# Kernel optimization log

Hardware: AMD Instinct MI355X
Metric: run time of the kernel (lower is better)

The kernel has to match this reference:

```python
import jax, jax.numpy as jnp
import numpy as np


def setup_inputs() -> dict:
    key = jax.random.key(0)
    k1, k2 = jax.random.split(key)
    B, T, D = 8, 2048, 2048
    layer_in = jax.random.normal(k1, (B, T, D), dtype=jnp.float32)
    # nn.Linear(2D, 2D): weight [out=2D, in=2D], bias [2D]
    W_gate = jax.random.normal(k2, (2 * D, 2 * D), dtype=jnp.float32) * 0.02
    b_gate = jnp.zeros((2 * D,), dtype=jnp.float32)
    return {"layer_in": layer_in, "W_gate": W_gate, "b_gate": b_gate}


def reference(layer_in, W_gate, b_gate):
    # Cumulative average: tril(ones)/row_index @ x  ==  cumsum(x)/[1..t]
    t = layer_in.shape[1]
    denom = jnp.arange(1, t + 1, dtype=layer_in.dtype)[:, None]  # (t, 1)
    average_out = jnp.cumsum(layer_in, axis=1) / denom  # (B, t, D)
    # Gating: Linear(2D -> 2D) on concat(x, avg), then chunk into two gates
    gating_in = jnp.concatenate([layer_in, average_out], axis=-1)  # (B, t, 2D)
    gates = jnp.einsum('btk,ok->bto', gating_in, W_gate) + b_gate  # (B, t, 2D)
    input_gate, forget_gate = jnp.split(gates, 2, axis=2)
    gating_out = (jax.nn.sigmoid(input_gate) * layer_in
                  + jax.nn.sigmoid(forget_gate) * average_out)
    return gating_out, average_out
```

## Files before the change

### kernel.cpp

```cpp
#include <hip/hip_runtime.h>
#include <hip/hip_bf16.h>


#define Bb 8
#define Tt 2048
#define Dd 2048
#define Mm (Bb * Tt)
#define Kk 4096
#define NTK 128
#define NC 32
#define CT 64

typedef __bf16 bf16x8 __attribute__((ext_vector_type(8)));
typedef float f32x16 __attribute__((ext_vector_type(16)));

__device__ __forceinline__ void gload16(const void* g, void* l) {
    __builtin_amdgcn_global_load_lds(
        (const __attribute__((address_space(1))) unsigned int*)g,
        (__attribute__((address_space(3))) unsigned int*)l, 16, 0, 0);
}

__global__ void wconv_kernel(const float* __restrict__ W,
                             unsigned short* __restrict__ Wb, long n) {
    long i = ((long)blockIdx.x * blockDim.x + threadIdx.x) * 4;
    long stride = (long)gridDim.x * blockDim.x * 4;
    for (; i < n; i += stride) {
        float4 v = *(const float4*)(W + i);
        __hip_bfloat16 a = __float2bfloat16(v.x);
        __hip_bfloat16 b = __float2bfloat16(v.y);
        __hip_bfloat16 c = __float2bfloat16(v.z);
        __hip_bfloat16 d = __float2bfloat16(v.w);
        ushort4 u;
        u.x = *(unsigned short*)&a; u.y = *(unsigned short*)&b;
        u.z = *(unsigned short*)&c; u.w = *(unsigned short*)&d;
        *(ushort4*)(Wb + i) = u;
    }
}

__global__ void ksum_kernel(const float* __restrict__ X, float* __restrict__ S) {
    int d = blockIdx.y * 256 + threadIdx.x;
    int bc = blockIdx.x;
    int b = bc >> 5, c = bc & 31;
    const float* p = X + ((long)(b * Tt + c * CT)) * Dd + d;
    float s = 0.f;
#pragma unroll 8
    for (int t = 0; t < CT; ++t) s += p[(long)t * Dd];
    S[(long)bc * Dd + d] = s;
}

__global__ void kscan_kernel(const float* __restrict__ X, const float* __restrict__ S,
                             float* __restrict__ AVG, unsigned short* __restrict__ Gin) {
    int d = blockIdx.y * 256 + threadIdx.x;
    int bc = blockIdx.x;
    int b = bc >> 5, c = bc & 31;
    const float* Sp = S + (long)(b * NC) * Dd + d;
    float run = 0.f;
    for (int cc = 0; cc < c; ++cc) run += Sp[(long)cc * Dd];
    const float* p = X + ((long)(b * Tt + c * CT)) * Dd + d;
    long row = (long)b * Tt + c * CT;
    for (int tt = 0; tt < CT; ++tt) {
        float x = p[(long)tt * Dd];
        run += x;
        float av = run / (float)(c * CT + tt + 1);
        long r = row + tt;
        AVG[r * Dd + d] = av;
        __hip_bfloat16 xb = __float2bfloat16(x);
        __hip_bfloat16 ab = __float2bfloat16(av);
        Gin[r * 4096 + d] = *(unsigned short*)&xb;
        Gin[r * 4096 + 2048 + d] = *(unsigned short*)&ab;
    }
}

#define MFMA32(va, vb, c_) c_ = __builtin_amdgcn_mfma_f32_32x32x16_bf16(va, vb, c_, 0, 0, 0)
#define RD(p_, i_) (*(const bf16x8*)((p_) + (i_) * 2048))

#define PH(t_, kk_, IA_, IB_)                                                   \
  {                                                                             \
    const int buf_ = (t_) & 3;                                                  \
    const char* pa_ = ((kk_) ? rA1 : rA0) + buf_ * 32768;                       \
    const char* pb_ = ((kk_) ? rB1 : rB0) + buf_ * 32768;                       \
    bf16x8 a0 = RD(pa_,0), a1 = RD(pa_,1), a2 = RD(pa_,2), a3 = RD(pa_,3);      \
    bf16x8 b0 = RD(pb_,0), b1 = RD(pb_,1);                                      \
    if (IA_) { char* nd_ = ldsb + (((t_)+3)&3)*32768 + woff;                    \
      const long ko_ = ((long)(t_)+3)*64;                                       \
      gload16(gA0 + ko_, nd_); gload16(gA1 + ko_, nd_ + 8192); }                \
    if (IB_) { char* nd_ = ldsb + (((t_)+3)&3)*32768 + 16384 + woff;            \
      const long ko_ = ((long)(t_)+3)*64;                                       \
      gload16(gB0 + ko_, nd_); gload16(gB1 + ko_, nd_ + 8192); }                \
    __builtin_amdgcn_s_barrier();                                               \
    __builtin_amdgcn_sched_barrier(0);                                          \
    __builtin_amdgcn_s_setprio(1);                                              \
    MFMA32(a0, b0, acc[0][0]); MFMA32(a0, b1, acc[0][1]);                       \
    MFMA32(a1, b0, acc[1][0]); MFMA32(a1, b1, acc[1][1]);                       \
    MFMA32(a2, b0, acc[2][0]); MFMA32(a2, b1, acc[2][1]);                       \
    MFMA32(a3, b0, acc[3][0]); MFMA32(a3, b1, acc[3][1]);                       \
    __builtin_amdgcn_s_setprio(0);                                              \
    __builtin_amdgcn_sched_barrier(0);                                          \
  }

#define BOUNDARY(N_)                                                            \
  asm volatile("s_waitcnt vmcnt(" #N_ ")" ::: "memory");                        \
  __builtin_amdgcn_s_barrier();                                                 \
  __builtin_amdgcn_sched_barrier(0);

__global__ __launch_bounds__(512, 2) void gemm32_kernel(
    const unsigned short* __restrict__ Gin,
    const unsigned short* __restrict__ Wb,
    const float* __restrict__ bias,
    const float* __restrict__ X,
    const float* __restrict__ AVG,
    float* __restrict__ OUT)
{
    __shared__ __attribute__((aligned(128))) char lds[131072];
    char* ldsb = (char*)lds;

    const int tid = threadIdx.x;
    const int w = tid >> 6, l = tid & 63;
    const int wm = w >> 2, wn = w & 3;
    const int la = l & 31;
    const int lk = l >> 5;
    const int woff = w * 1024;

    const int bid = blockIdx.x;
    const int batch = bid >> 8;
    const int rr = bid & 255;
    const int xcd = rr & 7;
    const int j = rr >> 3;
    const int nt = xcd * 2 + (j >> 4);
    const int mt = batch * 16 + (j & 15);
    const long m0 = (long)mt * 256;
    const int n0 = nt * 128;

    const int srow = tid >> 2;
    const int schunk = (tid & 3) ^ ((tid >> 3) & 3);
    const char* gA0 = (const char*)Gin + (m0 + srow) * 8192 + schunk * 16;
    const char* gA1 = gA0 + 128 * 8192;
    const long jr0 = n0 + ((srow >> 6) << 5) + (srow & 31) + (((srow >> 5) & 1) << 11);
    const int j1 = 128 + srow;
    const long jr1 = n0 + ((j1 >> 6) << 5) + (j1 & 31) + (((j1 >> 5) & 1) << 11);
    const char* gB0 = (const char*)Wb + jr0 * 8192 + schunk * 16;
    const char* gB1 = (const char*)Wb + jr1 * 8192 + schunk * 16;

    const int cb0 = ((lk ^ ((la >> 1) & 3))) * 16;
    const int cb1 = cb0 ^ 32;
    const char* rA0 = ldsb + (wm * 128 + la) * 64 + cb0;
    const char* rA1 = ldsb + (wm * 128 + la) * 64 + cb1;
    const char* rB0 = ldsb + 16384 + (wn * 64 + la) * 64 + cb0;
    const char* rB1 = ldsb + 16384 + (wn * 64 + la) * 64 + cb1;

    f32x16 acc[4][2] = {};

    {
        gload16(gA0,       ldsb + woff);
        gload16(gA1,       ldsb + 8192 + woff);
        gload16(gB0,       ldsb + 16384 + woff);
        gload16(gB1,       ldsb + 24576 + woff);
        gload16(gA0 + 64,  ldsb + 32768 + woff);
        gload16(gA1 + 64,  ldsb + 32768 + 8192 + woff);
        gload16(gB0 + 64,  ldsb + 32768 + 16384 + woff);
        gload16(gB1 + 64,  ldsb + 32768 + 24576 + woff);
        gload16(gA0 + 128, ldsb + 65536 + woff);
        gload16(gA1 + 128, ldsb + 65536 + 8192 + woff);
        gload16(gB0 + 128, ldsb + 65536 + 16384 + woff);
        gload16(gB1 + 128, ldsb + 65536 + 24576 + woff);
    }
    BOUNDARY(8);

#pragma unroll 1
    for (int t = 0; t < NTK - 3; ++t) {
        PH(t, 0, 1, 0);
        PH(t, 1, 0, 1);
        BOUNDARY(8);
    }
    PH(125, 0, 0, 0); PH(125, 1, 0, 0);
    BOUNDARY(4);
    PH(126, 0, 0, 0); PH(126, 1, 0, 0);
    BOUNDARY(0);
    PH(127, 0, 0, 0); PH(127, 1, 0, 0);

    const int d = n0 + wn * 32 + la;
    const float bi_ = bias[d];
    const float bf_ = bias[d + 2048];
#pragma unroll
    for (int mi = 0; mi < 4; ++mi) {
        const long rb = m0 + wm * 128 + mi * 32 + lk * 4;
        f32x16 ci = acc[mi][0];
        f32x16 cf = acc[mi][1];
#pragma unroll
        for (int q = 0; q < 16; ++q) {
            long row = rb + (q & 3) + 8 * (q >> 2);
            long idx = row * 2048 + d;
            float gi = ci[q] + bi_;
            float gf = cf[q] + bf_;
            float x = X[idx];
            float av = AVG[idx];
            float si = 1.f / (1.f + __expf(-gi));
            float sf = 1.f / (1.f + __expf(-gf));
            OUT[idx] = si * x + sf * av;
        }
    }
}

extern "C" void kernel_launch(void* const* d_in, const int* in_sizes, int n_in,
                              void* d_out, int out_size, void* d_ws, size_t ws_size,
                              hipStream_t stream) {
    const float* X = (const float*)d_in[0];
    const float* W = (const float*)d_in[1];
    const float* bias = (const float*)d_in[2];

    float* OUT = (float*)d_out;
    float* AVG = OUT + (long)Mm * Dd;

    char* ws = (char*)d_ws;
    unsigned short* Wb  = (unsigned short*)ws;
    unsigned short* Gin = (unsigned short*)(ws + 33554432);
    float* S = (float*)(ws + 33554432 + 134217728);

    wconv_kernel<<<2048, 256, 0, stream>>>(W, Wb, (long)Kk * Kk);
    ksum_kernel<<<dim3(Bb * NC, Dd / 256), 256, 0, stream>>>(X, S);
    kscan_kernel<<<dim3(Bb * NC, Dd / 256), 256, 0, stream>>>(X, S, AVG, Gin);
    gemm32_kernel<<<1024, 512, 0, stream>>>(Gin, Wb, bias, X, AVG, OUT);
}
```

Baseline: 690.0 us.

## Load B operand directly into registers, shrink LDS to 3-stage A buffer

The GEMM kernel stops staging the weight (B) tiles through LDS. Each wave now loads its B fragments straight from global memory into double-buffered registers one k-step ahead, and only the activation (A) tile goes through a 3-deep LDS ring. LDS use drops from 128KB to 48KB and the loop is unrolled by 6 with one barrier per k-tile. The aim is to cut LDS traffic and barriers and to allow more occupancy. The cost is that B global loads are no longer shared across the 2 waves that use the same B rows, which raises global and L2 traffic, and global latency is only hidden one step ahead.

```diff
diff --git a/kernel.cpp b/kernel.cpp
--- a/kernel.cpp
+++ b/kernel.cpp
@@ -74,36 +74,46 @@
 #define MFMA32(va, vb, c_) c_ = __builtin_amdgcn_mfma_f32_32x32x16_bf16(va, vb, c_, 0, 0, 0)
 #define RD(p_, i_) (*(const bf16x8*)((p_) + (i_) * 2048))
 
-#define PH(t_, kk_, IA_, IB_)                                                   \
+#define TILE(t_, buf_, bs_, IB_, IA_, NV_)                                      \
   {                                                                             \
-    const int buf_ = (t_) & 3;                                                  \
-    const char* pa_ = ((kk_) ? rA1 : rA0) + buf_ * 32768;                       \
-    const char* pb_ = ((kk_) ? rB1 : rB0) + buf_ * 32768;                       \
-    bf16x8 a0 = RD(pa_,0), a1 = RD(pa_,1), a2 = RD(pa_,2), a3 = RD(pa_,3);      \
-    bf16x8 b0 = RD(pb_,0), b1 = RD(pb_,1);                                      \
-    if (IA_) { char* nd_ = ldsb + (((t_)+3)&3)*32768 + woff;                    \
-      const long ko_ = ((long)(t_)+3)*64;                                       \
-      gload16(gA0 + ko_, nd_); gload16(gA1 + ko_, nd_ + 8192); }                \
-    if (IB_) { char* nd_ = ldsb + (((t_)+3)&3)*32768 + 16384 + woff;            \
-      const long ko_ = ((long)(t_)+3)*64;                                       \
-      gload16(gB0 + ko_, nd_); gload16(gB1 + ko_, nd_ + 8192); }                \
+    if (IB_) {                                                                  \
+      const long o_ = ((long)(t_) + 1) * 64;                                    \
+      breg[(bs_) ^ 1][0] = *(const bf16x8*)(pB0 + o_);                          \
+      breg[(bs_) ^ 1][1] = *(const bf16x8*)(pB0 + o_ + 32);                     \
+      breg[(bs_) ^ 1][2] = *(const bf16x8*)(pB1 + o_);                          \
+      breg[(bs_) ^ 1][3] = *(const bf16x8*)(pB1 + o_ + 32);                     \
+    }                                                                           \
+    if (IA_) {                                                                  \
+      char* nd_ = ldsb + (((t_) + 2) % 3) * 16384 + woff;                       \
+      const long ko_ = ((long)(t_) + 2) * 64;                                   \
+      gload16(gA0 + ko_, nd_); gload16(gA1 + ko_, nd_ + 8192);                  \
+    }                                                                           \
+    {                                                                           \
+      const char* pa_ = rA0 + (buf_) * 16384;                                   \
+      bf16x8 a0 = RD(pa_,0), a1 = RD(pa_,1), a2 = RD(pa_,2), a3 = RD(pa_,3);    \
+      __builtin_amdgcn_s_setprio(1);                                            \
+      MFMA32(a0, breg[bs_][0], acc[0][0]); MFMA32(a0, breg[bs_][2], acc[0][1]); \
+      MFMA32(a1, breg[bs_][0], acc[1][0]); MFMA32(a1, breg[bs_][2], acc[1][1]); \
+      MFMA32(a2, breg[bs_][0], acc[2][0]); MFMA32(a2, breg[bs_][2], acc[2][1]); \
+      MFMA32(a3, breg[bs_][0], acc[3][0]); MFMA32(a3, breg[bs_][2], acc[3][1]); \
+      __builtin_amdgcn_s_setprio(0);                                            \
+    }                                                                           \
+    {                                                                           \
+      const char* pa_ = rA1 + (buf_) * 16384;                                   \
+      bf16x8 a0 = RD(pa_,0), a1 = RD(pa_,1), a2 = RD(pa_,2), a3 = RD(pa_,3);    \
+      __builtin_amdgcn_s_setprio(1);                                            \
+      MFMA32(a0, breg[bs_][1], acc[0][0]); MFMA32(a0, breg[bs_][3], acc[0][1]); \
+      MFMA32(a1, breg[bs_][1], acc[1][0]); MFMA32(a1, breg[bs_][3], acc[1][1]); \
+      MFMA32(a2, breg[bs_][1], acc[2][0]); MFMA32(a2, breg[bs_][3], acc[2][1]); \
+      MFMA32(a3, breg[bs_][1], acc[3][0]); MFMA32(a3, breg[bs_][3], acc[3][1]); \
+      __builtin_amdgcn_s_setprio(0);                                            \
+    }                                                                           \
+    asm volatile("s_waitcnt vmcnt(" #NV_ ")" ::: "memory");                     \
     __builtin_amdgcn_s_barrier();                                               \
     __builtin_amdgcn_sched_barrier(0);                                          \
-    __builtin_amdgcn_s_setprio(1);                                              \
-    MFMA32(a0, b0, acc[0][0]); MFMA32(a0, b1, acc[0][1]);                       \
-    MFMA32(a1, b0, acc[1][0]); MFMA32(a1, b1, acc[1][1]);                       \
-    MFMA32(a2, b0, acc[2][0]); MFMA32(a2, b1, acc[2][1]);                       \
-    MFMA32(a3, b0, acc[3][0]); MFMA32(a3, b1, acc[3][1]);                       \
-    __builtin_amdgcn_s_setprio(0);                                              \
-    __builtin_amdgcn_sched_barrier(0);                                          \
   }
 
-#define BOUNDARY(N_)                                                            \
-  asm volatile("s_waitcnt vmcnt(" #N_ ")" ::: "memory");                        \
-  __builtin_amdgcn_s_barrier();                                                 \
-  __builtin_amdgcn_sched_barrier(0);
-
-__global__ __launch_bounds__(512, 2) void gemm32_kernel(
+__global__ __launch_bounds__(512, 2) void gemm32r_kernel(
     const unsigned short* __restrict__ Gin,
     const unsigned short* __restrict__ Wb,
     const float* __restrict__ bias,
@@ -111,7 +121,7 @@
     const float* __restrict__ AVG,
     float* __restrict__ OUT)
 {
-    __shared__ __attribute__((aligned(128))) char lds[131072];
+    __shared__ __attribute__((aligned(128))) char lds[49152];
     char* ldsb = (char*)lds;
 
     const int tid = threadIdx.x;
@@ -135,48 +145,41 @@
     const int schunk = (tid & 3) ^ ((tid >> 3) & 3);
     const char* gA0 = (const char*)Gin + (m0 + srow) * 8192 + schunk * 16;
     const char* gA1 = gA0 + 128 * 8192;
-    const long jr0 = n0 + ((srow >> 6) << 5) + (srow & 31) + (((srow >> 5) & 1) << 11);
-    const int j1 = 128 + srow;
-    const long jr1 = n0 + ((j1 >> 6) << 5) + (j1 & 31) + (((j1 >> 5) & 1) << 11);
-    const char* gB0 = (const char*)Wb + jr0 * 8192 + schunk * 16;
-    const char* gB1 = (const char*)Wb + jr1 * 8192 + schunk * 16;
+
+    const char* pB0 = (const char*)Wb + (long)(n0 + wn * 32 + la) * 8192 + lk * 16;
+    const char* pB1 = (const char*)Wb + (long)(n0 + wn * 32 + la + 2048) * 8192 + lk * 16;
 
     const int cb0 = ((lk ^ ((la >> 1) & 3))) * 16;
     const int cb1 = cb0 ^ 32;
     const char* rA0 = ldsb + (wm * 128 + la) * 64 + cb0;
     const char* rA1 = ldsb + (wm * 128 + la) * 64 + cb1;
-    const char* rB0 = ldsb + 16384 + (wn * 64 + la) * 64 + cb0;
-    const char* rB1 = ldsb + 16384 + (wn * 64 + la) * 64 + cb1;
 
     f32x16 acc[4][2] = {};
-
-    {
-        gload16(gA0,       ldsb + woff);
-        gload16(gA1,       ldsb + 8192 + woff);
-        gload16(gB0,       ldsb + 16384 + woff);
-        gload16(gB1,       ldsb + 24576 + woff);
-        gload16(gA0 + 64,  ldsb + 32768 + woff);
-        gload16(gA1 + 64,  ldsb + 32768 + 8192 + woff);
-        gload16(gB0 + 64,  ldsb + 32768 + 16384 + woff);
-        gload16(gB1 + 64,  ldsb + 32768 + 24576 + woff);
-        gload16(gA0 + 128, ldsb + 65536 + woff);
-        gload16(gA1 + 128, ldsb + 65536 + 8192 + woff);
-        gload16(gB0 + 128, ldsb + 65536 + 16384 + woff);
-        gload16(gB1 + 128, ldsb + 65536 + 24576 + woff);
-    }
-    BOUNDARY(8);
+    bf16x8 breg[2][4];
+
+    gload16(gA0,      ldsb + woff);
+    gload16(gA1,      ldsb + 8192 + woff);
+    gload16(gA0 + 64, ldsb + 16384 + woff);
+    gload16(gA1 + 64, ldsb + 16384 + 8192 + woff);
+    breg[0][0] = *(const bf16x8*)(pB0);
+    breg[0][1] = *(const bf16x8*)(pB0 + 32);
+    breg[0][2] = *(const bf16x8*)(pB1);
+    breg[0][3] = *(const bf16x8*)(pB1 + 32);
+    asm volatile("s_waitcnt vmcnt(0)" ::: "memory");
+    __builtin_amdgcn_s_barrier();
+    __builtin_amdgcn_sched_barrier(0);
 
 #pragma unroll 1
-    for (int t = 0; t < NTK - 3; ++t) {
-        PH(t, 0, 1, 0);
-        PH(t, 1, 0, 1);
-        BOUNDARY(8);
-    }
-    PH(125, 0, 0, 0); PH(125, 1, 0, 0);
-    BOUNDARY(4);
-    PH(126, 0, 0, 0); PH(126, 1, 0, 0);
-    BOUNDARY(0);
-    PH(127, 0, 0, 0); PH(127, 1, 0, 0);
+    for (int t = 0; t < 126; t += 6) {
+        TILE(t + 0, 0, 0, 1, 1, 2)
+        TILE(t + 1, 1, 1, 1, 1, 2)
+        TILE(t + 2, 2, 0, 1, 1, 2)
+        TILE(t + 3, 0, 1, 1, 1, 2)
+        TILE(t + 4, 1, 0, 1, 1, 2)
+        TILE(t + 5, 2, 1, 1, 1, 2)
+    }
+    TILE(126, 0, 0, 1, 0, 0)
+    TILE(127, 1, 1, 0, 0, 0)
 
     const int d = n0 + wn * 32 + la;
     const float bi_ = bias[d];
@@ -219,5 +222,5 @@
     wconv_kernel<<<2048, 256, 0, stream>>>(W, Wb, (long)Kk * Kk);
     ksum_kernel<<<dim3(Bb * NC, Dd / 256), 256, 0, stream>>>(X, S);
     kscan_kernel<<<dim3(Bb * NC, Dd / 256), 256, 0, stream>>>(X, S, AVG, Gin);
-    gemm32_kernel<<<1024, 512, 0, stream>>>(Gin, Wb, bias, X, AVG, OUT);
-}
+    gemm32r_kernel<<<1024, 512, 0, stream>>>(Gin, Wb, bias, X, AVG, OUT);
+}
```

New measurement: 998.5 us. 44.7% more time.

## Restructure GEMM main loop to double-buffered K=128 tiles with register ping-pong

Applied to the files above, without the earlier changes.

The GEMM pipeline changes from a 4-deep ring of K=64 LDS stages to two 64KB buffers holding K=128 tiles, with one barrier per tile. LDS fragment reads are ping-ponged between two register sets so the next reads overlap the current MFMA cluster. The epilogue now reads the bf16 copies of x and avg from Gin instead of the fp32 X and AVG arrays, which halves epilogue read traffic but loses precision in the output blend. Launch bounds drop the 2-blocks hint, and each tile now waits for vmcnt(0), so prefetch depth is reduced.

```diff
diff --git a/kernel.cpp b/kernel.cpp
--- a/kernel.cpp
+++ b/kernel.cpp
@@ -7,7 +7,6 @@
 #define Dd 2048
 #define Mm (Bb * Tt)
 #define Kk 4096
-#define NTK 128
 #define NC 32
 #define CT 64
 
@@ -72,43 +71,69 @@
 }
 
 #define MFMA32(va, vb, c_) c_ = __builtin_amdgcn_mfma_f32_32x32x16_bf16(va, vb, c_, 0, 0, 0)
-#define RD(p_, i_) (*(const bf16x8*)((p_) + (i_) * 2048))
-
-#define PH(t_, kk_, IA_, IB_)                                                   \
+#define SBAR __builtin_amdgcn_s_barrier()
+#define SCHB __builtin_amdgcn_sched_barrier(0)
+#define LGKM0 do { asm volatile("s_waitcnt lgkmcnt(0)" ::: "memory"); SCHB; } while (0)
+
+#define READ6(S_, pA_, pB_)                                                     \
+    S_##a0 = *(const bf16x8*)(pA_);                                             \
+    S_##a1 = *(const bf16x8*)((pA_) + 4096);                                    \
+    S_##a2 = *(const bf16x8*)((pA_) + 8192);                                    \
+    S_##a3 = *(const bf16x8*)((pA_) + 12288);                                   \
+    S_##b0 = *(const bf16x8*)(pB_);                                             \
+    S_##b1 = *(const bf16x8*)((pB_) + 4096);
+
+#define CLUST(S_)                                                               \
+    __builtin_amdgcn_s_setprio(1);                                              \
+    MFMA32(S_##a0, S_##b0, acc[0][0]); MFMA32(S_##a0, S_##b1, acc[0][1]);       \
+    MFMA32(S_##a1, S_##b0, acc[1][0]); MFMA32(S_##a1, S_##b1, acc[1][1]);       \
+    MFMA32(S_##a2, S_##b0, acc[2][0]); MFMA32(S_##a2, S_##b1, acc[2][1]);       \
+    MFMA32(S_##a3, S_##b0, acc[3][0]); MFMA32(S_##a3, S_##b1, acc[3][1]);       \
+    __builtin_amdgcn_s_setprio(0);
+
+#define STAGE8(nw_, ko_)                                                        \
+    gload16(gA0 + (ko_),           (nw_));                                      \
+    gload16(gA0 + 524288 + (ko_),  (nw_) + 8192);                               \
+    gload16(gA0 + 1048576 + (ko_), (nw_) + 16384);                              \
+    gload16(gA0 + 1572864 + (ko_), (nw_) + 24576);                              \
+    gload16(gB0 + (ko_),           (nw_) + 32768);                              \
+    gload16(gB0 + 262144 + (ko_),  (nw_) + 40960);                              \
+    gload16(gB0 + 524288 + (ko_),  (nw_) + 49152);                              \
+    gload16(gB0 + 786432 + (ko_),  (nw_) + 57344);
+
+#define TILE32(t_, bb_, STG_, RDX_)                                             \
   {                                                                             \
-    const int buf_ = (t_) & 3;                                                  \
-    const char* pa_ = ((kk_) ? rA1 : rA0) + buf_ * 32768;                       \
-    const char* pb_ = ((kk_) ? rB1 : rB0) + buf_ * 32768;                       \
-    bf16x8 a0 = RD(pa_,0), a1 = RD(pa_,1), a2 = RD(pa_,2), a3 = RD(pa_,3);      \
-    bf16x8 b0 = RD(pb_,0), b1 = RD(pb_,1);                                      \
-    if (IA_) { char* nd_ = ldsb + (((t_)+3)&3)*32768 + woff;                    \
-      const long ko_ = ((long)(t_)+3)*64;                                       \
-      gload16(gA0 + ko_, nd_); gload16(gA1 + ko_, nd_ + 8192); }                \
-    if (IB_) { char* nd_ = ldsb + (((t_)+3)&3)*32768 + 16384 + woff;            \
-      const long ko_ = ((long)(t_)+3)*64;                                       \
-      gload16(gB0 + ko_, nd_); gload16(gB1 + ko_, nd_ + 8192); }                \
-    __builtin_amdgcn_s_barrier();                                               \
-    __builtin_amdgcn_sched_barrier(0);                                          \
-    __builtin_amdgcn_s_setprio(1);                                              \
-    MFMA32(a0, b0, acc[0][0]); MFMA32(a0, b1, acc[0][1]);                       \
-    MFMA32(a1, b0, acc[1][0]); MFMA32(a1, b1, acc[1][1]);                       \
-    MFMA32(a2, b0, acc[2][0]); MFMA32(a2, b1, acc[2][1]);                       \
-    MFMA32(a3, b0, acc[3][0]); MFMA32(a3, b1, acc[3][1]);                       \
-    __builtin_amdgcn_s_setprio(0);                                              \
-    __builtin_amdgcn_sched_barrier(0);                                          \
+    const char* b_ = ldsb + (bb_);                                              \
+    const char* nb_ = ldsb + ((bb_) ^ 65536);                                   \
+    char* nw_ = ldsb + ((bb_) ^ 65536) + woff;                                  \
+    const long ko_ = ((long)(t_) + 1) * 128;                                    \
+         \
+    LGKM0;                                                                      \
+    READ6(q, b_ + rAk1, b_ + rBk1)                                              \
+    if (STG_) { STAGE8(nw_, ko_) }                                              \
+    CLUST(p)                                                                    \
+                                   \
+    LGKM0;                                                                      \
+    READ6(p, b_ + rAk2, b_ + rBk2)                                              \
+    CLUST(q)                                                                    \
+                                   \
+    LGKM0;                                                                      \
+    READ6(q, b_ + rAk3, b_ + rBk3)                                              \
+    CLUST(p)                                                                    \
+                     \
+    asm volatile("s_waitcnt vmcnt(0) lgkmcnt(0)" ::: "memory");                 \
+    SBAR; SCHB;                                                                 \
+                        \
+    if (RDX_) { READ6(p, nb_ + rAk0, nb_ + rBk0) }                              \
+    SCHB;                                                                       \
+    CLUST(q)                                                                    \
+    SCHB;                                                                       \
   }
 
-#define BOUNDARY(N_)                                                            \
-  asm volatile("s_waitcnt vmcnt(" #N_ ")" ::: "memory");                        \
-  __builtin_amdgcn_s_barrier();                                                 \
-  __builtin_amdgcn_sched_barrier(0);
-
-__global__ __launch_bounds__(512, 2) void gemm32_kernel(
+__global__ __launch_bounds__(512) void gemm32s_kernel(
     const unsigned short* __restrict__ Gin,
     const unsigned short* __restrict__ Wb,
     const float* __restrict__ bias,
-    const float* __restrict__ X,
-    const float* __restrict__ AVG,
     float* __restrict__ OUT)
 {
     __shared__ __attribute__((aligned(128))) char lds[131072];
@@ -131,52 +156,41 @@
     const long m0 = (long)mt * 256;
     const int n0 = nt * 128;
 
-    const int srow = tid >> 2;
-    const int schunk = (tid & 3) ^ ((tid >> 3) & 3);
-    const char* gA0 = (const char*)Gin + (m0 + srow) * 8192 + schunk * 16;
-    const char* gA1 = gA0 + 128 * 8192;
-    const long jr0 = n0 + ((srow >> 6) << 5) + (srow & 31) + (((srow >> 5) & 1) << 11);
-    const int j1 = 128 + srow;
-    const long jr1 = n0 + ((j1 >> 6) << 5) + (j1 & 31) + (((j1 >> 5) & 1) << 11);
-    const char* gB0 = (const char*)Wb + jr0 * 8192 + schunk * 16;
-    const char* gB1 = (const char*)Wb + jr1 * 8192 + schunk * 16;
-
-    const int cb0 = ((lk ^ ((la >> 1) & 3))) * 16;
-    const int cb1 = cb0 ^ 32;
-    const char* rA0 = ldsb + (wm * 128 + la) * 64 + cb0;
-    const char* rA1 = ldsb + (wm * 128 + la) * 64 + cb1;
-    const char* rB0 = ldsb + 16384 + (wn * 64 + la) * 64 + cb0;
-    const char* rB1 = ldsb + 16384 + (wn * 64 + la) * 64 + cb1;
+    const int srow8 = tid >> 3;
+    const int sq = (tid & 7) ^ (srow8 & 7);
+    const char* gA0 = (const char*)Gin + (m0 + srow8) * 8192 + sq * 16;
+    const char* gB0 = (const char*)Wb
+        + ((long)(n0 + (srow8 & 31) + ((srow8 >> 5) << 11))) * 8192 + sq * 16;
+
+    const int c0 = (lk ^ (la & 7)) << 4;
+    const int rAbase = (wm * 128 + la) * 128 + c0;
+    const int rBbase = 32768 + (wn * 64 + la) * 128 + c0;
+    const int rAk0 = rAbase;        const int rBk0 = rBbase;
+    const int rAk1 = rAbase ^ 32;   const int rBk1 = rBbase ^ 32;
+    const int rAk2 = rAbase ^ 64;   const int rBk2 = rBbase ^ 64;
+    const int rAk3 = rAbase ^ 96;   const int rBk3 = rBbase ^ 96;
 
     f32x16 acc[4][2] = {};
 
+    bf16x8 pa0, pa1, pa2, pa3, pb0, pb1;
+    bf16x8 qa0, qa1, qa2, qa3, qb0, qb1;
+
     {
-        gload16(gA0,       ldsb + woff);
-        gload16(gA1,       ldsb + 8192 + woff);
-        gload16(gB0,       ldsb + 16384 + woff);
-        gload16(gB1,       ldsb + 24576 + woff);
-        gload16(gA0 + 64,  ldsb + 32768 + woff);
-        gload16(gA1 + 64,  ldsb + 32768 + 8192 + woff);
-        gload16(gB0 + 64,  ldsb + 32768 + 16384 + woff);
-        gload16(gB1 + 64,  ldsb + 32768 + 24576 + woff);
-        gload16(gA0 + 128, ldsb + 65536 + woff);
-        gload16(gA1 + 128, ldsb + 65536 + 8192 + woff);
-        gload16(gB0 + 128, ldsb + 65536 + 16384 + woff);
-        gload16(gB1 + 128, ldsb + 65536 + 24576 + woff);
-    }
-    BOUNDARY(8);
+        char* w0 = ldsb + woff;
+        STAGE8(w0, 0)
+    }
+    asm volatile("s_waitcnt vmcnt(0)" ::: "memory");
+    SBAR; SCHB;
+    READ6(p, ldsb + rAk0, ldsb + rBk0)
+    SCHB;
 
 #pragma unroll 1
-    for (int t = 0; t < NTK - 3; ++t) {
-        PH(t, 0, 1, 0);
-        PH(t, 1, 0, 1);
-        BOUNDARY(8);
-    }
-    PH(125, 0, 0, 0); PH(125, 1, 0, 0);
-    BOUNDARY(4);
-    PH(126, 0, 0, 0); PH(126, 1, 0, 0);
-    BOUNDARY(0);
-    PH(127, 0, 0, 0); PH(127, 1, 0, 0);
+    for (int t = 0; t < 62; t += 2) {
+        TILE32(t,     0,     1, 1)
+        TILE32(t + 1, 65536, 1, 1)
+    }
+    TILE32(62, 0,     1, 1)
+    TILE32(63, 65536, 0, 0)
 
     const int d = n0 + wn * 32 + la;
     const float bi_ = bias[d];
@@ -187,16 +201,17 @@
         f32x16 ci = acc[mi][0];
         f32x16 cf = acc[mi][1];
 #pragma unroll
-        for (int q = 0; q < 16; ++q) {
-            long row = rb + (q & 3) + 8 * (q >> 2);
-            long idx = row * 2048 + d;
-            float gi = ci[q] + bi_;
-            float gf = cf[q] + bf_;
-            float x = X[idx];
-            float av = AVG[idx];
+        for (int qq = 0; qq < 16; ++qq) {
+            long row = rb + (qq & 3) + 8 * (qq >> 2);
+            unsigned int ux = Gin[row * 4096 + d];
+            unsigned int ua = Gin[row * 4096 + 2048 + d];
+            union { unsigned int u; float f; } cx, ca;
+            cx.u = ux << 16; ca.u = ua << 16;
+            float gi = ci[qq] + bi_;
+            float gf = cf[qq] + bf_;
             float si = 1.f / (1.f + __expf(-gi));
             float sf = 1.f / (1.f + __expf(-gf));
-            OUT[idx] = si * x + sf * av;
+            OUT[row * 2048 + d] = si * cx.f + sf * ca.f;
         }
     }
 }
@@ -219,5 +234,5 @@
     wconv_kernel<<<2048, 256, 0, stream>>>(W, Wb, (long)Kk * Kk);
     ksum_kernel<<<dim3(Bb * NC, Dd / 256), 256, 0, stream>>>(X, S);
     kscan_kernel<<<dim3(Bb * NC, Dd / 256), 256, 0, stream>>>(X, S, AVG, Gin);
-    gemm32_kernel<<<1024, 512, 0, stream>>>(Gin, Wb, bias, X, AVG, OUT);
-}
+    gemm32s_kernel<<<1024, 512, 0, stream>>>(Gin, Wb, bias, OUT);
+}
```

Result: faster. 641.6 us (-7.0%).
